# Kernel tuning notes

Hardware: AMD Instinct MI355X
Metric: run time of the kernel (lower is better)

## Reference

```python
import jax, jax.numpy as jnp
import numpy as np

HEADS = 4
BN_EPS = 1e-5


def _linear_attention(x, heads):
    # x: [B, L, C]; per-head linear attention: softmax(Q,dim=feat) @ (softmax(K,dim=seq)^T @ V)
    B, L, C = x.shape
    dh = C // heads
    h = x.reshape(B, L, heads, dh)
    q = jax.nn.softmax(h, axis=-1)          # softmax over feature dim (dim=2 in torch)
    k = jax.nn.softmax(h, axis=1)           # softmax over sequence dim (dim=1 in torch)
    kv = jnp.einsum('blhd,blhe->bhde', k, h)   # [B, H, dh, dh]
    out = jnp.einsum('blhd,bhde->blhe', q, kv) # [B, L, H, dh]
    return out.reshape(B, L, C)


def setup_inputs() -> dict:
    key = jax.random.key(0)
    ks = jax.random.split(key, 10)
    B, C, L, DOUT, NB = 32, 32, 16384, 10, 3
    s = 0.1
    return {
        'x': jax.random.normal(ks[0], (B, C, L), jnp.float32),
        'fcW1': jax.random.normal(ks[1], (NB, C, C), jnp.float32) * s,
        'fcb1': jax.random.normal(ks[2], (NB, C), jnp.float32) * s,
        'fcW2': jax.random.normal(ks[3], (NB, C, C), jnp.float32) * s,
        'fcb2': jax.random.normal(ks[4], (NB, C), jnp.float32) * s,
        'Wh': jax.random.normal(ks[5], (C, C), jnp.float32) * s,
        'bh': jax.random.normal(ks[6], (C,), jnp.float32) * s,
        'bn_gamma': jnp.ones((C,), jnp.float32),
        'bn_beta': jnp.zeros((C,), jnp.float32),
        'bn_mean': jnp.zeros((C,), jnp.float32),
        'bn_var': jnp.ones((C,), jnp.float32),
        'Wf': jax.random.normal(ks[7], (C, DOUT), jnp.float32) * s,
        'bf': jax.random.normal(ks[8], (DOUT,), jnp.float32) * s,
    }


def reference(x, fcW1, fcb1, fcW2, fcb2, Wh, bh, bn_gamma, bn_beta, bn_mean, bn_var, Wf, bf):
    gelu = lambda t: jax.nn.gelu(t, approximate=False)  # torch default GELU is exact erf
    h = jnp.transpose(x, (0, 2, 1))  # [B, C, L] -> [B, L, C]
    n_blocks = fcW1.shape[0]
    for i in range(n_blocks):
        h = _linear_attention(h, HEADS)
        h = gelu(h @ fcW1[i] + fcb1[i])
        h = gelu(h @ fcW2[i] + fcb2[i])
    pooled = jnp.mean(h, axis=1)  # AdaptiveAvgPool1d(1) over L -> [B, C]
    y = pooled @ Wh + bh
    y = (y - bn_mean) * jax.lax.rsqrt(bn_var + BN_EPS) * bn_gamma + bn_beta  # BatchNorm1d (eval)
    y = gelu(y)
    return y @ Wf + bf
```

## Files before the change

kernel.cpp:

```cpp
#include <hip/hip_runtime.h>
#include <cstddef>

#define B_ 32
#define C_ 32
#define L_ 16384
#define H_ 4
#define DH_ 8
#define NB_ 3
#define DOUT_ 10
#define SEG_ 512
#define S_ (L_/SEG_)

#define TILE 256
#define AST  40

typedef _Float16 f16_t;
typedef _Float16 f16x2 __attribute__((ext_vector_type(2)));
typedef _Float16 f16x4 __attribute__((ext_vector_type(4)));
typedef _Float16 f16x8 __attribute__((ext_vector_type(8)));
typedef float    f32x4 __attribute__((ext_vector_type(4)));

__device__ __forceinline__ float gelu_f(float x){
    const float z  = fabsf(x) * 0.70710678118654752440f;
    const float t  = __builtin_amdgcn_rcpf(fmaf(0.47047f, z, 1.0f));
    const float e  = __expf(-z * z);
    float p = fmaf(t, 0.7478556f, -0.0958798f);
    p = fmaf(t, p, 0.3480242f);
    const float erfz = 1.0f - p * t * e;
    const float phi  = fmaf(copysignf(erfz, x), 0.5f, 0.5f);
    return x * phi;
}

#define RED_MAX32(v) do{ v = fmaxf(v, __shfl_xor(v,1));  v = fmaxf(v, __shfl_xor(v,2)); \
                         v = fmaxf(v, __shfl_xor(v,4));  v = fmaxf(v, __shfl_xor(v,8)); \
                         v = fmaxf(v, __shfl_xor(v,16)); }while(0)
#define RED_SUM32(v) do{ v += __shfl_xor(v,1);  v += __shfl_xor(v,2); \
                         v += __shfl_xor(v,4);  v += __shfl_xor(v,8); \
                         v += __shfl_xor(v,16); }while(0)

template<typename T>
__global__ __launch_bounds__(256) void stats_kernel(const T* __restrict__ h,
                                                    float* __restrict__ part,
                                                    float* __restrict__ zpool){
    const int seg = blockIdx.x;
    const int hd  = blockIdx.y;
    const int b   = blockIdx.z;
    const int t   = threadIdx.x;
    const int d   = t >> 5;
    const int j   = t & 31;

    __shared__ float tile[8][SEG_];
    __shared__ float sm[8];

    if (zpool != nullptr && blockIdx.x == 0 && blockIdx.y == 0 && blockIdx.z == 0)
        for (int i = t; i < B_*C_; i += 256) zpool[i] = 0.0f;

    const T* hb = h + (size_t)b * ((size_t)C_*L_) + (size_t)(hd*DH_)*L_ + (size_t)seg*SEG_;

    if constexpr (sizeof(T) == 4){
        for (int f = t; f < 8*SEG_/4; f += 256){
            const int row = f >> 7;
            const int c4  = (f & 127) << 2;
            *(f32x4*)&tile[row][c4] = *(const f32x4*)&hb[(size_t)row*L_ + c4];
        }
    } else {
        for (int f = t; f < 8*SEG_/8; f += 256){
            const int row = f >> 6;
            const int c8  = (f & 63) << 3;
            const f16x8 v = *(const f16x8*)&hb[(size_t)row*L_ + c8];
            f32x4 lo = {(float)v[0], (float)v[1], (float)v[2], (float)v[3]};
            f32x4 hi = {(float)v[4], (float)v[5], (float)v[6], (float)v[7]};
            *(f32x4*)&tile[row][c8]     = lo;
            *(f32x4*)&tile[row][c8 + 4] = hi;
        }
    }
    __syncthreads();

    float m = -INFINITY;
    #pragma unroll
    for (int i = 0; i < SEG_/32; i++) m = fmaxf(m, tile[d][j + 32*i]);
    RED_MAX32(m);
    if (j == 0) sm[d] = m;
    const float m_d = m;

    float s = 0.0f;
    float kv[8];
    #pragma unroll
    for (int e = 0; e < 8; e++) kv[e] = 0.0f;
    #pragma unroll
    for (int i = 0; i < SEG_/32; i++){
        const int k = j + 32*i;
        const float ek = __expf(tile[d][k] - m_d);
        s += ek;
        #pragma unroll
        for (int e = 0; e < 8; e++) kv[e] = fmaf(ek, tile[e][k], kv[e]);
    }
    RED_SUM32(s);
    #pragma unroll
    for (int e = 0; e < 8; e++){ RED_SUM32(kv[e]); }
    __syncthreads();

    float* po = part + (size_t)((b*H_ + hd)*S_ + seg) * 80;
    if (j == 0){
        po[8 + d] = s;
        #pragma unroll
        for (int e = 0; e < 8; e++) po[16 + d*8 + e] = kv[e];
    }
    if (t < 8) po[t] = sm[t];
}

template<bool FIRST, bool LAST>
__global__ __launch_bounds__(256)
__attribute__((amdgpu_waves_per_eu(3, 4)))
void block_kernel(const void* hin,
                  f16_t* hout,
                  const float* __restrict__ part,
                  const float* __restrict__ W1,
                  const float* __restrict__ b1,
                  const float* __restrict__ W2,
                  const float* __restrict__ b2,
                  float* __restrict__ pooled){
    __shared__ __align__(16) f16_t Ash[TILE*AST];
    __shared__ f16_t Bsh1[32*AST];
    __shared__ f16_t Bsh2[32*AST];
    __shared__ float sb1[32], sb2[32];
    __shared__ float kvsh[256];
    __shared__ float pool[32];

    const int tid = threadIdx.x;
    const int b   = blockIdx.y;
    const int l0  = blockIdx.x * TILE;
    const int l   = l0 + tid;
    const size_t base = (size_t)b * ((size_t)C_*L_);

    float h[32];
    if constexpr (FIRST){
        const float* hf = (const float*)hin;
        #pragma unroll
        for (int c = 0; c < 32; c++) h[c] = hf[base + (size_t)c*L_ + l];
    } else {
        const f16_t* hh = (const f16_t*)hin;
        #pragma unroll
        for (int c = 0; c < 32; c++) h[c] = (float)hh[base + (size_t)c*L_ + l];
    }

    for (int i = tid; i < 1024; i += 256){
        const int k = i >> 5, n = i & 31;
        Bsh2[n*AST + k] = (f16_t)W2[i];
    }
    if (tid < 32){ sb1[tid] = b1[tid]; sb2[tid] = b2[tid]; }
    if (LAST && tid < 32) pool[tid] = 0.0f;

    {
        const int hh_t = tid >> 6;
        const int tt   = tid & 63;
        const int dd   = tt >> 3;
        const float* pp = part + (size_t)(b*H_ + hh_t) * S_ * 80;
        float M = -INFINITY;
        for (int s2 = 0; s2 < S_; s2++) M = fmaxf(M, pp[s2*80 + dd]);
        float ssum = 0.0f, kvs = 0.0f;
        for (int s2 = 0; s2 < S_; s2++){
            const float sc = __expf(pp[s2*80 + dd] - M);
            ssum = fmaf(pp[s2*80 + 8  + dd], sc, ssum);
            kvs  = fmaf(pp[s2*80 + 16 + tt], sc, kvs);
        }
        kvsh[tid] = kvs / ssum;
    }

    #pragma unroll
    for (int hh = 0; hh < 4; hh++){
        float mq = h[hh*8];
        #pragma unroll
        for (int d2 = 1; d2 < 8; d2++) mq = fmaxf(mq, h[hh*8 + d2]);
        float es[8]; float qs = 0.f;
        #pragma unroll
        for (int d2 = 0; d2 < 8; d2++){ es[d2] = __expf(h[hh*8 + d2] - mq); qs += es[d2]; }
        const float inv = __builtin_amdgcn_rcpf(qs);
        f16x8 pv;
        #pragma unroll
        for (int d2 = 0; d2 < 8; d2++) pv[d2] = (f16_t)(es[d2] * inv);
        *(f16x8*)&Ash[tid*AST + hh*8] = pv;
    }
    __syncthreads();

    {
        const int row = tid >> 3;
        const int hh2 = row >> 3;
        const int q   = tid & 7;
        float kvr[8];
        #pragma unroll
        for (int e = 0; e < 8; e++) kvr[e] = kvsh[row*8 + e];
        f32x4 acc = {0.f, 0.f, 0.f, 0.f};
        #pragma unroll
        for (int e = 0; e < 8; e++){
            const f32x4 w = *(const f32x4*)&W1[(hh2*8 + e)*32 + q*4];
            acc += kvr[e] * w;
        }
        #pragma unroll
        for (int j2 = 0; j2 < 4; j2++)
            Bsh1[(q*4 + j2)*AST + row] = (f16_t)acc[j2];
    }
    __syncthreads();

    const int wv   = tid >> 6;
    const int lane = tid & 63;
    const int lr   = lane & 15;
    const int lk   = lane >> 4;
    const f32x4 zero = {0.f, 0.f, 0.f, 0.f};

    f16x8 a[4], bw[2];
    f32x4 d[8];

    #pragma unroll
    for (int mt = 0; mt < 4; mt++)
        a[mt] = *(const f16x8*)&Ash[(wv*64 + mt*16 + lr)*AST + lk*8];
    #pragma unroll
    for (int nt = 0; nt < 2; nt++)
        bw[nt] = *(const f16x8*)&Bsh1[(nt*16 + lr)*AST + lk*8];
    #pragma unroll
    for (int nt = 0; nt < 2; nt++)
        #pragma unroll
        for (int mt = 0; mt < 4; mt++)
            d[nt*4+mt] = __builtin_amdgcn_mfma_f32_16x16x32_f16(a[mt], bw[nt], zero, 0, 0, 0);

    #pragma unroll
    for (int nt = 0; nt < 2; nt++){
        const float bias = sb1[nt*16 + lr];
        #pragma unroll
        for (int mt = 0; mt < 4; mt++)
            #pragma unroll
            for (int r = 0; r < 4; r++){
                const float v = gelu_f(d[nt*4+mt][r] + bias);
                Ash[(wv*64 + mt*16 + lk*4 + r)*AST + (nt*16 + lr)] = (f16_t)v;
            }
    }

    #pragma unroll
    for (int mt = 0; mt < 4; mt++)
        a[mt] = *(const f16x8*)&Ash[(wv*64 + mt*16 + lr)*AST + lk*8];
    #pragma unroll
    for (int nt = 0; nt < 2; nt++)
        bw[nt] = *(const f16x8*)&Bsh2[(nt*16 + lr)*AST + lk*8];
    #pragma unroll
    for (int nt = 0; nt < 2; nt++)
        #pragma unroll
        for (int mt = 0; mt < 4; mt++)
            d[nt*4+mt] = __builtin_amdgcn_mfma_f32_16x16x32_f16(a[mt], bw[nt], zero, 0, 0, 0);

    #pragma unroll
    for (int nt = 0; nt < 2; nt++){
        const float bias = sb2[nt*16 + lr];
        #pragma unroll
        for (int mt = 0; mt < 4; mt++)
            #pragma unroll
            for (int r = 0; r < 4; r++)
                d[nt*4+mt][r] = gelu_f(d[nt*4+mt][r] + bias);
    }

    if (!LAST){
        #pragma unroll
        for (int nt = 0; nt < 2; nt++)
            #pragma unroll
            for (int mt = 0; mt < 4; mt++){
                const f32x4 dv = d[nt*4+mt];
                f16x4 hv = { (f16_t)dv[0], (f16_t)dv[1], (f16_t)dv[2], (f16_t)dv[3] };
                *(f16x4*)&hout[base + (size_t)(nt*16 + lr)*L_
                               + l0 + wv*64 + mt*16 + lk*4] = hv;
            }
    } else {
        #pragma unroll
        for (int nt = 0; nt < 2; nt++){
            float ps = 0.f;
            #pragma unroll
            for (int mt = 0; mt < 4; mt++)
                ps += d[nt*4+mt][0] + d[nt*4+mt][1] + d[nt*4+mt][2] + d[nt*4+mt][3];
            atomicAdd(&pool[nt*16 + lr], ps);
        }
        __syncthreads();
        if (tid < 32) atomicAdd(&pooled[b*32 + tid], pool[tid]);
    }
}

__global__ __launch_bounds__(1024) void head_kernel(const float* __restrict__ pooled,
                                                    const float* __restrict__ Wh,
                                                    const float* __restrict__ bh,
                                                    const float* __restrict__ gam,
                                                    const float* __restrict__ bet,
                                                    const float* __restrict__ mean,
                                                    const float* __restrict__ var,
                                                    const float* __restrict__ Wf,
                                                    const float* __restrict__ bf,
                                                    float* __restrict__ out){
    __shared__ float y2[32][32];
    const int t = threadIdx.x;
    const int b = t >> 5, c = t & 31;
    float a = bh[c];
    const float invL = 1.0f / (float)L_;
    #pragma unroll
    for (int d = 0; d < 32; d++) a += (pooled[b*32 + d] * invL) * Wh[d*32 + c];
    a = (a - mean[c]) * rsqrtf(var[c] + 1e-5f) * gam[c] + bet[c];
    y2[b][c] = gelu_f(a);
    __syncthreads();
    if (t < B_*DOUT_){
        const int b2 = t / DOUT_, j = t % DOUT_;
        float r = bf[j];
        #pragma unroll
        for (int c2 = 0; c2 < 32; c2++) r += y2[b2][c2] * Wf[c2*DOUT_ + j];
        out[t] = r;
    }
}

extern "C" void kernel_launch(void* const* d_in, const int* in_sizes, int n_in,
                              void* d_out, int out_size, void* d_ws, size_t ws_size,
                              hipStream_t stream){
    (void)in_sizes; (void)n_in; (void)out_size; (void)ws_size;
    const float* x    = (const float*)d_in[0];
    const float* fW1  = (const float*)d_in[1];
    const float* fb1  = (const float*)d_in[2];
    const float* fW2  = (const float*)d_in[3];
    const float* fb2  = (const float*)d_in[4];
    const float* Wh   = (const float*)d_in[5];
    const float* bh   = (const float*)d_in[6];
    const float* gam  = (const float*)d_in[7];
    const float* bet  = (const float*)d_in[8];
    const float* mean = (const float*)d_in[9];
    const float* var  = (const float*)d_in[10];
    const float* Wf   = (const float*)d_in[11];
    const float* bf   = (const float*)d_in[12];
    float* out = (float*)d_out;

    f16_t* hbuf   = (f16_t*)d_ws;
    float* part   = (float*)((char*)d_ws + (size_t)B_*C_*L_*2);
    float* pooled = part + (size_t)B_*H_*S_*80;

    dim3 sgrid(S_, H_, B_);
    dim3 bgrid(L_/TILE, B_);

    stats_kernel<float><<<sgrid, 256, 0, stream>>>(x, part, nullptr);
    block_kernel<true, false><<<bgrid, 256, 0, stream>>>(x, hbuf, part,
        fW1, fb1, fW2, fb2, nullptr);
    stats_kernel<f16_t><<<sgrid, 256, 0, stream>>>(hbuf, part, nullptr);
    block_kernel<false, false><<<bgrid, 256, 0, stream>>>(hbuf, hbuf, part,
        fW1 + C_*C_, fb1 + C_, fW2 + C_*C_, fb2 + C_, nullptr);
    stats_kernel<f16_t><<<sgrid, 256, 0, stream>>>(hbuf, part, pooled);
    block_kernel<false, true><<<bgrid, 256, 0, stream>>>(hbuf, nullptr, part,
        fW1 + 2*C_*C_, fb1 + 2*C_, fW2 + 2*C_*C_, fb2 + 2*C_, pooled);

    head_kernel<<<1, 1024, 0, stream>>>(pooled, Wh, bh, gam, bet, mean, var, Wf, bf, out);
}
```

Baseline: 274.9 us.

## Load activations directly in MFMA fragment layout and parallelize kv reduction

```diff
diff --git a/kernel.cpp b/kernel.cpp
--- a/kernel.cpp
+++ b/kernel.cpp
@@ -120,103 +120,119 @@
                   const float* __restrict__ W2,
                   const float* __restrict__ b2,
                   float* __restrict__ pooled){
-    __shared__ __align__(16) f16_t Ash[TILE*AST];
-    __shared__ f16_t Bsh1[32*AST];
-    __shared__ f16_t Bsh2[32*AST];
-    __shared__ float sb1[32], sb2[32];
-    __shared__ float kvsh[256];
-    __shared__ float pool[32];
-
-    const int tid = threadIdx.x;
-    const int b   = blockIdx.y;
-    const int l0  = blockIdx.x * TILE;
-    const int l   = l0 + tid;
+    __shared__ __align__(16) f16_t AO[TILE*AST];
+
+    const int tid  = threadIdx.x;
+    const int b    = blockIdx.y;
+    const int l0   = blockIdx.x * TILE;
     const size_t base = (size_t)b * ((size_t)C_*L_);
-
-    float h[32];
-    if constexpr (FIRST){
-        const float* hf = (const float*)hin;
-        #pragma unroll
-        for (int c = 0; c < 32; c++) h[c] = hf[base + (size_t)c*L_ + l];
-    } else {
-        const f16_t* hh = (const f16_t*)hin;
-        #pragma unroll
-        for (int c = 0; c < 32; c++) h[c] = (float)hh[base + (size_t)c*L_ + l];
-    }
-
-    for (int i = tid; i < 1024; i += 256){
-        const int k = i >> 5, n = i & 31;
-        Bsh2[n*AST + k] = (f16_t)W2[i];
-    }
-    if (tid < 32){ sb1[tid] = b1[tid]; sb2[tid] = b2[tid]; }
-    if (LAST && tid < 32) pool[tid] = 0.0f;
-
-    {
-        const int hh_t = tid >> 6;
-        const int tt   = tid & 63;
-        const int dd   = tt >> 3;
-        const float* pp = part + (size_t)(b*H_ + hh_t) * S_ * 80;
-        float M = -INFINITY;
-        for (int s2 = 0; s2 < S_; s2++) M = fmaxf(M, pp[s2*80 + dd]);
-        float ssum = 0.0f, kvs = 0.0f;
-        for (int s2 = 0; s2 < S_; s2++){
-            const float sc = __expf(pp[s2*80 + dd] - M);
-            ssum = fmaf(pp[s2*80 + 8  + dd], sc, ssum);
-            kvs  = fmaf(pp[s2*80 + 16 + tt], sc, kvs);
-        }
-        kvsh[tid] = kvs / ssum;
-    }
-
-    #pragma unroll
-    for (int hh = 0; hh < 4; hh++){
-        float mq = h[hh*8];
-        #pragma unroll
-        for (int d2 = 1; d2 < 8; d2++) mq = fmaxf(mq, h[hh*8 + d2]);
-        float es[8]; float qs = 0.f;
-        #pragma unroll
-        for (int d2 = 0; d2 < 8; d2++){ es[d2] = __expf(h[hh*8 + d2] - mq); qs += es[d2]; }
-        const float inv = __builtin_amdgcn_rcpf(qs);
-        f16x8 pv;
-        #pragma unroll
-        for (int d2 = 0; d2 < 8; d2++) pv[d2] = (f16_t)(es[d2] * inv);
-        *(f16x8*)&Ash[tid*AST + hh*8] = pv;
-    }
-    __syncthreads();
-
-    {
-        const int row = tid >> 3;
-        const int hh2 = row >> 3;
-        const int q   = tid & 7;
-        float kvr[8];
-        #pragma unroll
-        for (int e = 0; e < 8; e++) kvr[e] = kvsh[row*8 + e];
-        f32x4 acc = {0.f, 0.f, 0.f, 0.f};
-        #pragma unroll
-        for (int e = 0; e < 8; e++){
-            const f32x4 w = *(const f32x4*)&W1[(hh2*8 + e)*32 + q*4];
-            acc += kvr[e] * w;
-        }
-        #pragma unroll
-        for (int j2 = 0; j2 < 4; j2++)
-            Bsh1[(q*4 + j2)*AST + row] = (f16_t)acc[j2];
-    }
-    __syncthreads();
 
     const int wv   = tid >> 6;
     const int lane = tid & 63;
     const int lr   = lane & 15;
     const int lk   = lane >> 4;
+    const int posb = l0 + wv*64 + lr;
+
+    float h[4][8];
+    if constexpr (FIRST){
+        const float* hf = (const float*)hin;
+        #pragma unroll
+        for (int j = 0; j < 8; j++)
+            #pragma unroll
+            for (int mt = 0; mt < 4; mt++)
+                h[mt][j] = hf[base + (size_t)(lk*8 + j)*L_ + posb + mt*16];
+    } else {
+        const f16_t* hh = (const f16_t*)hin;
+        #pragma unroll
+        for (int j = 0; j < 8; j++)
+            #pragma unroll
+            for (int mt = 0; mt < 4; mt++)
+                h[mt][j] = (float)hh[base + (size_t)(lk*8 + j)*L_ + posb + mt*16];
+    }
+
+    for (int i = tid; i < 1024; i += 256){
+        const int k = i >> 5, n = i & 31;
+        AO[(size_t)(128 + n*4 + (k >> 3))*AST + 32 + (k & 7)] = (f16_t)W2[i];
+    }
+    float bias1[2], bias2[2];
+    #pragma unroll
+    for (int nt = 0; nt < 2; nt++){ bias1[nt] = b1[nt*16 + lr]; bias2[nt] = b2[nt*16 + lr]; }
+
+    f16x8 a[4];
+    #pragma unroll
+    for (int mt = 0; mt < 4; mt++){
+        float mq = h[mt][0];
+        #pragma unroll
+        for (int j = 1; j < 8; j++) mq = fmaxf(mq, h[mt][j]);
+        float es[8]; float qs = 0.f;
+        #pragma unroll
+        for (int j = 0; j < 8; j++){ es[j] = __expf(h[mt][j] - mq); qs += es[j]; }
+        const float inv = __builtin_amdgcn_rcpf(qs);
+        #pragma unroll
+        for (int j = 0; j < 8; j++) a[mt][j] = (f16_t)(es[j] * inv);
+    }
+
+    const int row = tid >> 3;
+    const int qq  = tid & 7;
+    const int hdm = row >> 3, dm = row & 7;
+    {
+        const float* pp = part + (size_t)(b*H_ + hdm) * S_ * 80;
+        float pm[4];
+        #pragma unroll
+        for (int t4 = 0; t4 < 4; t4++) pm[t4] = pp[(qq + 8*t4)*80 + dm];
+        float M = fmaxf(fmaxf(pm[0], pm[1]), fmaxf(pm[2], pm[3]));
+        float ss = 0.f;
+        float kvr[8];
+        #pragma unroll
+        for (int e = 0; e < 8; e++) kvr[e] = 0.f;
+        #pragma unroll
+        for (int t4 = 0; t4 < 4; t4++){
+            const int s = qq + 8*t4;
+            const float sc = __expf(pm[t4] - M);
+            ss = fmaf(pp[s*80 + 8 + dm], sc, ss);
+            const f32x4 k0 = *(const f32x4*)&pp[s*80 + 16 + dm*8];
+            const f32x4 k1 = *(const f32x4*)&pp[s*80 + 16 + dm*8 + 4];
+            #pragma unroll
+            for (int e = 0; e < 4; e++){
+                kvr[e]   = fmaf(k0[e], sc, kvr[e]);
+                kvr[4+e] = fmaf(k1[e], sc, kvr[4+e]);
+            }
+        }
+        #pragma unroll
+        for (int off = 1; off < 8; off <<= 1){
+            const float Mo  = __shfl_xor(M, off);
+            const float sso = __shfl_xor(ss, off);
+            const float Mn  = fmaxf(M, Mo);
+            const float sa  = __expf(M - Mn), sb = __expf(Mo - Mn);
+            ss = ss*sa + sso*sb;
+            #pragma unroll
+            for (int e = 0; e < 8; e++){
+                const float ko = __shfl_xor(kvr[e], off);
+                kvr[e] = kvr[e]*sa + ko*sb;
+            }
+            M = Mn;
+        }
+        const float iss = 1.0f / ss;
+
+        f32x4 acc = {0.f, 0.f, 0.f, 0.f};
+        #pragma unroll
+        for (int e = 0; e < 8; e++){
+            const f32x4 w = *(const f32x4*)&W1[(hdm*8 + e)*32 + qq*4];
+            acc += kvr[e] * w;
+        }
+        #pragma unroll
+        for (int j2 = 0; j2 < 4; j2++)
+            AO[(size_t)((qq*4 + j2)*4 + hdm)*AST + 32 + dm] = (f16_t)(acc[j2] * iss);
+    }
+    __syncthreads();
+
     const f32x4 zero = {0.f, 0.f, 0.f, 0.f};
-
-    f16x8 a[4], bw[2];
+    f16x8 bw[2];
     f32x4 d[8];
 
     #pragma unroll
-    for (int mt = 0; mt < 4; mt++)
-        a[mt] = *(const f16x8*)&Ash[(wv*64 + mt*16 + lr)*AST + lk*8];
-    #pragma unroll
-    for (int nt = 0; nt < 2; nt++)
-        bw[nt] = *(const f16x8*)&Bsh1[(nt*16 + lr)*AST + lk*8];
+    for (int nt = 0; nt < 2; nt++)
+        bw[nt] = *(const f16x8*)&AO[(size_t)((nt*16 + lr)*4 + lk)*AST + 32];
     #pragma unroll
     for (int nt = 0; nt < 2; nt++)
         #pragma unroll
@@ -225,37 +241,35 @@
 
     #pragma unroll
     for (int nt = 0; nt < 2; nt++){
-        const float bias = sb1[nt*16 + lr];
         #pragma unroll
         for (int mt = 0; mt < 4; mt++)
             #pragma unroll
             for (int r = 0; r < 4; r++){
-                const float v = gelu_f(d[nt*4+mt][r] + bias);
-                Ash[(wv*64 + mt*16 + lk*4 + r)*AST + (nt*16 + lr)] = (f16_t)v;
+                const float v = gelu_f(d[nt*4+mt][r] + bias1[nt]);
+                AO[(size_t)(wv*64 + mt*16 + lk*4 + r)*AST + (nt*16 + lr)] = (f16_t)v;
             }
     }
 
+    f16x8 a2[4];
     #pragma unroll
     for (int mt = 0; mt < 4; mt++)
-        a[mt] = *(const f16x8*)&Ash[(wv*64 + mt*16 + lr)*AST + lk*8];
-    #pragma unroll
-    for (int nt = 0; nt < 2; nt++)
-        bw[nt] = *(const f16x8*)&Bsh2[(nt*16 + lr)*AST + lk*8];
+        a2[mt] = *(const f16x8*)&AO[(size_t)(wv*64 + mt*16 + lr)*AST + lk*8];
+    #pragma unroll
+    for (int nt = 0; nt < 2; nt++)
+        bw[nt] = *(const f16x8*)&AO[(size_t)(128 + (nt*16 + lr)*4 + lk)*AST + 32];
     #pragma unroll
     for (int nt = 0; nt < 2; nt++)
         #pragma unroll
         for (int mt = 0; mt < 4; mt++)
-            d[nt*4+mt] = __builtin_amdgcn_mfma_f32_16x16x32_f16(a[mt], bw[nt], zero, 0, 0, 0);
-
-    #pragma unroll
-    for (int nt = 0; nt < 2; nt++){
-        const float bias = sb2[nt*16 + lr];
+            d[nt*4+mt] = __builtin_amdgcn_mfma_f32_16x16x32_f16(a2[mt], bw[nt], zero, 0, 0, 0);
+
+    #pragma unroll
+    for (int nt = 0; nt < 2; nt++)
         #pragma unroll
         for (int mt = 0; mt < 4; mt++)
             #pragma unroll
             for (int r = 0; r < 4; r++)
-                d[nt*4+mt][r] = gelu_f(d[nt*4+mt][r] + bias);
-    }
+                d[nt*4+mt][r] = gelu_f(d[nt*4+mt][r] + bias2[nt]);
 
     if (!LAST){
         #pragma unroll
@@ -274,10 +288,10 @@
             #pragma unroll
             for (int mt = 0; mt < 4; mt++)
                 ps += d[nt*4+mt][0] + d[nt*4+mt][1] + d[nt*4+mt][2] + d[nt*4+mt][3];
-            atomicAdd(&pool[nt*16 + lr], ps);
-        }
-        __syncthreads();
-        if (tid < 32) atomicAdd(&pooled[b*32 + tid], pool[tid]);
+            ps += __shfl_xor(ps, 16);
+            ps += __shfl_xor(ps, 32);
+            if (lk == 0) atomicAdd(&pooled[b*32 + nt*16 + lr], ps);
+        }
     }
 }
 
```

Measured after the change: 270.1 us. Within noise of the previous version (-1.7%).
